# Performance work log

Hardware: AMD Instinct MI355X
Metric: run time of the kernel (lower is better)

Reference implementation:

```python
import jax, jax.numpy as jnp
import numpy as np

N_X, N_U, N_Y = 256, 32, 32
BATCH, T = 16, 8192
LAM_MIN, LAM_MAX = 0.9, 0.995
B_SCALE, D_SCALE = 0.25, 0.25


def setup_inputs() -> dict:
    key = jax.random.key(0)
    k = jax.random.split(key, 6)
    # Orthogonal Q via QR of a random Gaussian matrix (as in the torch module)
    M = jax.random.normal(k[0], (N_X, N_X), dtype=jnp.float32)
    Q, _ = jnp.linalg.qr(M)
    lam = LAM_MIN + (LAM_MAX - LAM_MIN) * jax.random.uniform(k[1], (N_X,), dtype=jnp.float32)
    Bmat = B_SCALE * jax.random.normal(k[2], (N_X, N_U), dtype=jnp.float32)
    # C picks out the first n_y coordinates (C[i, i] = 1)
    C = jnp.eye(N_Y, N_X, dtype=jnp.float32)
    D = D_SCALE * jax.random.normal(k[3], (N_Y, N_U), dtype=jnp.float32)
    x0 = jax.random.normal(k[4], (BATCH, N_X), dtype=jnp.float32)
    u = jax.random.normal(k[5], (BATCH, T, N_U), dtype=jnp.float32)
    return {"x0": x0, "u": u, "Q": Q, "lam": lam, "Bmat": Bmat, "C": C, "D": D}


def _diag_scan(lam, v):
    """Diagonal linear recurrence x_t = lam * x_{t-1} + v_t (x_0 folded into v[:, 0]).

    lam: (N,), v: (B, T, N) -> states x_1..x_T of shape (B, T, N).
    """
    a = jnp.broadcast_to(lam, v.shape)

    def op(l, r):
        a1, b1 = l
        a2, b2 = r
        return a1 * a2, a2 * b1 + b2

    return jax.lax.associative_scan(op, (a, v), axis=1)[1]


def reference(x0, u, Q, lam, Bmat, C, D):
    Bz = Q.T @ Bmat            # (n_x, n_u) modal input matrix
    Cz = C @ Q                 # (n_y, n_x) modal output matrix
    z0 = x0 @ Q                # (B, n_x)   modal initial state
    v = jnp.einsum('btu,nu->btn', u, Bz)   # (B, T, n_x)
    v = v.at[:, 0].add(lam * z0)            # fold lam * z0 into first step
    z_next = _diag_scan(lam, v)             # (B, T, n_x) = z_1..z_T
    # y_t uses z_t for t = 0..T-1 (states[:, :-1] in the original)
    z_prev = jnp.concatenate([z0[:, None, :], z_next[:, :-1]], axis=1)
    y = jnp.einsum('btn,yn->bty', z_prev, Cz) + jnp.einsum('btu,yu->bty', u, D)
    return y
```

## Files before the change

kernel.cpp:

```cpp
#include <hip/hip_runtime.h>

typedef _Float16 half4_t __attribute__((ext_vector_type(4)));
typedef _Float16 half8_t __attribute__((ext_vector_type(8)));
typedef float f32x4 __attribute__((ext_vector_type(4)));

constexpr int NX = 256, NU = 32, NY = 32, BATCH = 16, T = 8192;
constexpr int NC = 64, L = 128;
constexpr int SUBT = 32, NSUB = L / SUBT;
constexpr int KW = NX + NU;
constexpr int VP = 40;
constexpr int ZP = 264;
constexpr int POOLSZ = NX * VP;

__global__ __launch_bounds__(256) void k_pre(
    const float* __restrict__ x0, const float* __restrict__ Q,
    const float* __restrict__ Bm, const float* __restrict__ C,
    const float* __restrict__ D,
    _Float16* __restrict__ Bzh, _Float16* __restrict__ Wh, float* __restrict__ z0)
{
    int o = blockIdx.x * 64 + (threadIdx.x >> 2);
    int p = threadIdx.x & 3;
    if (o >= 20480) {
        if (p == 0) {
            int g = o - 20480, iy = g >> 5, j = g & 31;
            Wh[iy * KW + NX + j] = (_Float16)D[iy * NU + j];
        }
        return;
    }
    float s = 0.f;
    int k0 = p * 64;
    if (o < 8192) {
        int n = o >> 5, j = o & 31;
        for (int k = k0; k < k0 + 64; ++k) s = fmaf(Q[k * NX + n], Bm[k * NU + j], s);
    } else if (o < 16384) {
        int g = o - 8192; int iy = g >> 8, nn = g & 255;
        for (int k = k0; k < k0 + 64; ++k) s = fmaf(C[iy * NX + k], Q[k * NX + nn], s);
    } else {
        int g = o - 16384; int b = g >> 8, nn = g & 255;
        for (int k = k0; k < k0 + 64; ++k) s = fmaf(x0[b * NX + k], Q[k * NX + nn], s);
    }
    s += __shfl_xor(s, 1);
    s += __shfl_xor(s, 2);
    if (p == 0) {
        if (o < 8192) {
            Bzh[o] = (_Float16)s;
        } else if (o < 16384) {
            int g = o - 8192; int iy = g >> 8, nn = g & 255;
            Wh[iy * KW + nn] = (_Float16)s;
        } else {
            z0[o - 16384] = s;
        }
    }
}

__global__ __launch_bounds__(256) void k_phase1(
    const float* __restrict__ u, const float* __restrict__ lam,
    const _Float16* __restrict__ Bzh, float* __restrict__ S)
{
    __shared__ __align__(16) _Float16 ut[2][SUBT][32];

    const int b = blockIdx.x >> 6, c = blockIdx.x & 63, tid = threadIdx.x;
    const int w = tid >> 6, lane = tid & 63, m16 = lane & 15, quad = lane >> 4;

    half8_t bfrag[4];
    #pragma unroll
    for (int i = 0; i < 4; ++i)
        bfrag[i] = *(const half8_t*)&Bzh[((4 * w + i) * 16 + m16) * NU + quad * 8];

    float wr[4][4], wt16[4], l32[4], acc[4];
    #pragma unroll
    for (int i = 0; i < 4; ++i) {
        float la = lam[(4 * w + i) * 16 + m16];
        float p2 = la * la, p4 = p2 * p2, p8 = p4 * p4, p16 = p8 * p8;
        float inv1 = 1.0f / la;
        float inv4 = (inv1 * inv1) * (inv1 * inv1);
        float pq = 1.0f;
        if (quad & 1) pq *= inv4;
        if (quad & 2) pq *= inv4 * inv4;
        float w0 = (p16 * p8 * p4 * p2 * la) * pq;
        wr[i][0] = w0;
        wr[i][1] = w0 * inv1;
        wr[i][2] = wr[i][1] * inv1;
        wr[i][3] = wr[i][2] * inv1;
        wt16[i] = 1.0f / p16;
        l32[i] = p16 * p16;
        acc[i] = 0.f;
    }

    const float* ug = u + ((size_t)(b * T) + (size_t)c * L) * NU;

    for (int sub = 0; sub < NSUB; ++sub) {
        {
            float4 uu = *(const float4*)(ug + (size_t)sub * SUBT * NU + tid * 4);
            int tr = tid >> 3, cb = ((tid & 7) * 4 + (tr & 3) * 8) & 31;
            half4_t h; h.x = (_Float16)uu.x; h.y = (_Float16)uu.y;
            h.z = (_Float16)uu.z; h.w = (_Float16)uu.w;
            *(half4_t*)&ut[sub & 1][tr][cb] = h;
        }
        __syncthreads();
        int rot = (m16 & 3) * 8;
        half8_t af0 = *(const half8_t*)&ut[sub & 1][m16][(quad * 8 + rot) & 31];
        half8_t af1 = *(const half8_t*)&ut[sub & 1][16 + m16][(quad * 8 + rot) & 31];
        #pragma unroll
        for (int i = 0; i < 4; ++i) {
            f32x4 z4 = {0.f, 0.f, 0.f, 0.f};
            f32x4 v0 = __builtin_amdgcn_mfma_f32_16x16x32_f16(af0, bfrag[i], z4, 0, 0, 0);
            f32x4 v1 = __builtin_amdgcn_mfma_f32_16x16x32_f16(af1, bfrag[i], z4, 0, 0, 0);
            float s0 = wr[i][0] * v0[0] + wr[i][1] * v0[1] + wr[i][2] * v0[2] + wr[i][3] * v0[3];
            float s1 = wr[i][0] * v1[0] + wr[i][1] * v1[1] + wr[i][2] * v1[2] + wr[i][3] * v1[3];
            acc[i] = fmaf(l32[i], acc[i], fmaf(wt16[i], s1, s0));
        }
    }
    #pragma unroll
    for (int i = 0; i < 4; ++i) {
        acc[i] += __shfl_xor(acc[i], 16);
        acc[i] += __shfl_xor(acc[i], 32);
    }
    float out = quad == 0 ? acc[0] : quad == 1 ? acc[1] : quad == 2 ? acc[2] : acc[3];
    S[(size_t)blockIdx.x * NX + (4 * w + quad) * 16 + m16] = out;
}

__global__ __launch_bounds__(256) void k_phase3(
    const float* __restrict__ u, const float* __restrict__ lam,
    const _Float16* __restrict__ Bzh, const _Float16* __restrict__ Wh,
    const float* __restrict__ S, const float* __restrict__ z0,
    float* __restrict__ y)
{
    __shared__ __align__(16) _Float16 ut[2][SUBT][32];
    __shared__ __align__(16) _Float16 pool[POOLSZ];
    __shared__ float pvec[NX];

    const int b = blockIdx.x >> 6, c = blockIdx.x & 63, tid = threadIdx.x;
    const int w = tid >> 6, lane = tid & 63, m16 = lane & 15, quad = lane >> 4;
    const int tw = w & 1, yw = w >> 1;

    {
        float la = lam[tid], lamL = la;
        #pragma unroll
        for (int i = 0; i < 7; ++i) lamL *= lamL;
        const float* Sb = S + (size_t)(b * NC) * NX;
        float pv = 0.f, wgt = 1.f;
        for (int cc = c - 1; cc >= 0; --cc) {
            pv = fmaf(wgt, Sb[(size_t)cc * NX + tid], pv);
            wgt *= lamL;
        }
        pvec[tid] = fmaf(wgt, z0[b * NX + tid], pv);
    }

    half8_t bfrag[4];
    #pragma unroll
    for (int i = 0; i < 4; ++i)
        bfrag[i] = *(const half8_t*)&Bzh[((4 * w + i) * 16 + m16) * NU + quad * 8];
    half8_t wfrag[9];
    #pragma unroll
    for (int kk = 0; kk < 9; ++kk)
        wfrag[kk] = *(const half8_t*)&Wh[(yw * 16 + m16) * KW + kk * 32 + quad * 8];
    half8_t triA[2];
    #pragma unroll
    for (int tt = 0; tt < 2; ++tt) {
        #pragma unroll
        for (int j = 0; j < 8; ++j)
            triA[tt][j] = (_Float16)((quad * 8 + j < tt * 16 + m16) ? 1.f : 0.f);
    }

    float lamn[4], inv1[4], iq[4], i16p[4], fq[4], f16p[4], l32[4], p[4];
    #pragma unroll
    for (int i = 0; i < 4; ++i) {
        int ni = (4 * w + i) * 16 + m16;
        float la = lam[ni];
        lamn[i] = la;
        float p2 = la * la, p4 = p2 * p2, p8 = p4 * p4, p16 = p8 * p8;
        float iv = 1.0f / la;
        inv1[i] = iv;
        float iv4 = (iv * iv) * (iv * iv);
        float pqi = 1.0f, pqf = 1.0f;
        if (quad & 1) { pqi *= iv4; pqf *= p4; }
        if (quad & 2) { pqi *= iv4 * iv4; pqf *= p8; }
        iq[i] = iv * pqi;
        fq[i] = pqf;
        i16p[i] = 1.0f / p16;
        f16p[i] = p16;
        l32[i] = p16 * p16;
    }
    __syncthreads();
    #pragma unroll
    for (int i = 0; i < 4; ++i)
        p[i] = pvec[(4 * w + i) * 16 + m16];

    const float* ug = u + ((size_t)(b * T) + (size_t)c * L) * NU;
    float* yg = y + ((size_t)(b * T) + (size_t)c * L) * NY;
    const int rot = (m16 & 3) * 8;

    for (int sub = 0; sub < NSUB; ++sub) {
        {
            float4 uu = *(const float4*)(ug + (size_t)sub * SUBT * NU + tid * 4);
            int tr = tid >> 3, cb = ((tid & 7) * 4 + (tr & 3) * 8) & 31;
            half4_t h; h.x = (_Float16)uu.x; h.y = (_Float16)uu.y;
            h.z = (_Float16)uu.z; h.w = (_Float16)uu.w;
            *(half4_t*)&ut[sub & 1][tr][cb] = h;
        }
        __syncthreads();

        half8_t af0 = *(const half8_t*)&ut[sub & 1][m16][(quad * 8 + rot) & 31];
        half8_t af1 = *(const half8_t*)&ut[sub & 1][16 + m16][(quad * 8 + rot) & 31];
        float partial[4];
        #pragma unroll
        for (int i = 0; i < 4; ++i) {
            int ni = (4 * w + i) * 16 + m16;
            f32x4 z4 = {0.f, 0.f, 0.f, 0.f};
            f32x4 v0 = __builtin_amdgcn_mfma_f32_16x16x32_f16(af0, bfrag[i], z4, 0, 0, 0);
            f32x4 v1 = __builtin_amdgcn_mfma_f32_16x16x32_f16(af1, bfrag[i], z4, 0, 0, 0);
            float ps = 0.f;
            float sc = iq[i];
            half4_t h0, h1;
            #pragma unroll
            for (int r = 0; r < 4; ++r) {
                float a0 = v0[r] * sc;
                float a1 = v1[r] * (sc * i16p[i]);
                ps += a0 + a1;
                h0[r] = (_Float16)a0;
                h1[r] = (_Float16)a1;
                sc *= inv1[i];
            }
            partial[i] = ps;
            *(half4_t*)&pool[ni * VP + quad * 4] = h0;
            *(half4_t*)&pool[ni * VP + 16 + quad * 4] = h1;
        }
        __syncthreads();

        f32x4 zp0[4], zp1[4];
        #pragma unroll
        for (int i = 0; i < 4; ++i) {
            int ni = (4 * w + i) * 16 + m16;
            half8_t bV = *(const half8_t*)&pool[ni * VP + quad * 8];
            f32x4 z4 = {0.f, 0.f, 0.f, 0.f};
            zp0[i] = __builtin_amdgcn_mfma_f32_16x16x32_f16(triA[0], bV, z4, 0, 0, 0);
            zp1[i] = __builtin_amdgcn_mfma_f32_16x16x32_f16(triA[1], bV, z4, 0, 0, 0);
        }
        __syncthreads();

        #pragma unroll
        for (int i = 0; i < 4; ++i) {
            int ni = (4 * w + i) * 16 + m16;
            float f = fq[i];
            #pragma unroll
            for (int r = 0; r < 4; ++r) {
                float zv0 = f * (p[i] + zp0[i][r]);
                float zv1 = (f * f16p[i]) * (p[i] + zp1[i][r]);
                pool[(quad * 4 + r) * ZP + ni] = (_Float16)zv0;
                pool[(16 + quad * 4 + r) * ZP + ni] = (_Float16)zv1;
                f *= lamn[i];
            }
        }
        #pragma unroll
        for (int i = 0; i < 4; ++i) {
            float ps = partial[i];
            ps += __shfl_xor(ps, 16);
            ps += __shfl_xor(ps, 32);
            p[i] = l32[i] * (p[i] + ps);
        }
        __syncthreads();

        f32x4 acc = {0.f, 0.f, 0.f, 0.f};
        #pragma unroll
        for (int kk = 0; kk < 8; ++kk) {
            half8_t az = *(const half8_t*)&pool[(tw * 16 + m16) * ZP + kk * 32 + quad * 8];
            acc = __builtin_amdgcn_mfma_f32_16x16x32_f16(az, wfrag[kk], acc, 0, 0, 0);
        }
        {
            half8_t au = *(const half8_t*)&ut[sub & 1][tw * 16 + m16][(quad * 8 + rot) & 31];
            acc = __builtin_amdgcn_mfma_f32_16x16x32_f16(au, wfrag[8], acc, 0, 0, 0);
        }
        #pragma unroll
        for (int r = 0; r < 4; ++r)
            yg[(size_t)(sub * SUBT + tw * 16 + quad * 4 + r) * NY + yw * 16 + m16] = acc[r];
    }
}

extern "C" void kernel_launch(void* const* d_in, const int* in_sizes, int n_in,
                              void* d_out, int out_size, void* d_ws, size_t ws_size,
                              hipStream_t stream) {
    (void)in_sizes; (void)n_in; (void)out_size; (void)ws_size;
    const float* x0  = (const float*)d_in[0];
    const float* u   = (const float*)d_in[1];
    const float* Q   = (const float*)d_in[2];
    const float* lam = (const float*)d_in[3];
    const float* Bm  = (const float*)d_in[4];
    const float* C   = (const float*)d_in[5];
    const float* D   = (const float*)d_in[6];
    float* y = (float*)d_out;

    char* ws = (char*)d_ws;
    _Float16* Bzh = (_Float16*)(ws);
    _Float16* Wh  = (_Float16*)(ws + 16384);
    float*    z0  = (float*)(ws + 34816);
    float*    S   = (float*)(ws + 51200);

    k_pre   <<<336, 256, 0, stream>>>(x0, Q, Bm, C, D, Bzh, Wh, z0);
    k_phase1<<<BATCH * NC, 256, 0, stream>>>(u, lam, Bzh, S);
    k_phase3<<<BATCH * NC, 256, 0, stream>>>(u, lam, Bzh, Wh, S, z0, y);
}
```

Baseline: 129.9 us.

## Replace triangular-MFMA prefix sum with register/shuffle scan and exp2 carry weights

```diff
diff --git a/kernel.cpp b/kernel.cpp
--- a/kernel.cpp
+++ b/kernel.cpp
@@ -8,9 +8,7 @@
 constexpr int NC = 64, L = 128;
 constexpr int SUBT = 32, NSUB = L / SUBT;
 constexpr int KW = NX + NU;
-constexpr int VP = 40;
 constexpr int ZP = 264;
-constexpr int POOLSZ = NX * VP;
 
 __global__ __launch_bounds__(256) void k_pre(
     const float* __restrict__ x0, const float* __restrict__ Q,
@@ -127,7 +125,7 @@
     float* __restrict__ y)
 {
     __shared__ __align__(16) _Float16 ut[2][SUBT][32];
-    __shared__ __align__(16) _Float16 pool[POOLSZ];
+    __shared__ __align__(16) _Float16 zt[SUBT][ZP];
     __shared__ float pvec[NX];
 
     const int b = blockIdx.x >> 6, c = blockIdx.x & 63, tid = threadIdx.x;
@@ -135,16 +133,16 @@
     const int tw = w & 1, yw = w >> 1;
 
     {
-        float la = lam[tid], lamL = la;
-        #pragma unroll
-        for (int i = 0; i < 7; ++i) lamL *= lamL;
-        const float* Sb = S + (size_t)(b * NC) * NX;
-        float pv = 0.f, wgt = 1.f;
-        for (int cc = c - 1; cc >= 0; --cc) {
-            pv = fmaf(wgt, Sb[(size_t)cc * NX + tid], pv);
-            wgt *= lamL;
-        }
-        pvec[tid] = fmaf(wgt, z0[b * NX + tid], pv);
+        float la = lam[tid];
+        float l2L = 128.0f * __log2f(la);
+        const float* Sb = S + (size_t)(b * NC) * NX + tid;
+        float pv = 0.f;
+        #pragma unroll 8
+        for (int k = 0; k < c; ++k) {
+            float wgt = exp2f((float)k * l2L);
+            pv = fmaf(wgt, Sb[(size_t)(c - 1 - k) * NX], pv);
+        }
+        pvec[tid] = fmaf(exp2f((float)c * l2L), z0[b * NX + tid], pv);
     }
 
     half8_t bfrag[4];
@@ -155,13 +153,6 @@
     #pragma unroll
     for (int kk = 0; kk < 9; ++kk)
         wfrag[kk] = *(const half8_t*)&Wh[(yw * 16 + m16) * KW + kk * 32 + quad * 8];
-    half8_t triA[2];
-    #pragma unroll
-    for (int tt = 0; tt < 2; ++tt) {
-        #pragma unroll
-        for (int j = 0; j < 8; ++j)
-            triA[tt][j] = (_Float16)((quad * 8 + j < tt * 16 + m16) ? 1.f : 0.f);
-    }
 
     float lamn[4], inv1[4], iq[4], i16p[4], fq[4], f16p[4], l32[4], p[4];
     #pragma unroll
@@ -203,68 +194,52 @@
 
         half8_t af0 = *(const half8_t*)&ut[sub & 1][m16][(quad * 8 + rot) & 31];
         half8_t af1 = *(const half8_t*)&ut[sub & 1][16 + m16][(quad * 8 + rot) & 31];
-        float partial[4];
         #pragma unroll
         for (int i = 0; i < 4; ++i) {
             int ni = (4 * w + i) * 16 + m16;
             f32x4 z4 = {0.f, 0.f, 0.f, 0.f};
             f32x4 v0 = __builtin_amdgcn_mfma_f32_16x16x32_f16(af0, bfrag[i], z4, 0, 0, 0);
             f32x4 v1 = __builtin_amdgcn_mfma_f32_16x16x32_f16(af1, bfrag[i], z4, 0, 0, 0);
-            float ps = 0.f;
+            float a0[4], a1[4];
             float sc = iq[i];
-            half4_t h0, h1;
             #pragma unroll
             for (int r = 0; r < 4; ++r) {
-                float a0 = v0[r] * sc;
-                float a1 = v1[r] * (sc * i16p[i]);
-                ps += a0 + a1;
-                h0[r] = (_Float16)a0;
-                h1[r] = (_Float16)a1;
+                a0[r] = v0[r] * sc;
+                a1[r] = v1[r] * (sc * i16p[i]);
                 sc *= inv1[i];
             }
-            partial[i] = ps;
-            *(half4_t*)&pool[ni * VP + quad * 4] = h0;
-            *(half4_t*)&pool[ni * VP + 16 + quad * 4] = h1;
-        }
-        __syncthreads();
-
-        f32x4 zp0[4], zp1[4];
-        #pragma unroll
-        for (int i = 0; i < 4; ++i) {
-            int ni = (4 * w + i) * 16 + m16;
-            half8_t bV = *(const half8_t*)&pool[ni * VP + quad * 8];
-            f32x4 z4 = {0.f, 0.f, 0.f, 0.f};
-            zp0[i] = __builtin_amdgcn_mfma_f32_16x16x32_f16(triA[0], bV, z4, 0, 0, 0);
-            zp1[i] = __builtin_amdgcn_mfma_f32_16x16x32_f16(triA[1], bV, z4, 0, 0, 0);
-        }
-        __syncthreads();
-
-        #pragma unroll
-        for (int i = 0; i < 4; ++i) {
-            int ni = (4 * w + i) * 16 + m16;
+            float e0[4], e1[4];
+            e0[0] = 0.f; e0[1] = a0[0]; e0[2] = e0[1] + a0[1]; e0[3] = e0[2] + a0[2];
+            float S40 = e0[3] + a0[3];
+            e1[0] = 0.f; e1[1] = a1[0]; e1[2] = e1[1] + a1[1]; e1[3] = e1[2] + a1[2];
+            float S41 = e1[3] + a1[3];
+            float incl0 = S40;
+            float t0 = __shfl_up(incl0, 16); if (quad >= 1) incl0 += t0;
+            t0 = __shfl_up(incl0, 32);       if (quad >= 2) incl0 += t0;
+            float excl0 = incl0 - S40;
+            float total0 = __shfl(incl0, 48 + m16);
+            float incl1 = S41;
+            float t1 = __shfl_up(incl1, 16); if (quad >= 1) incl1 += t1;
+            t1 = __shfl_up(incl1, 32);       if (quad >= 2) incl1 += t1;
+            float excl1 = incl1 - S41;
+            float total1 = __shfl(incl1, 48 + m16);
             float f = fq[i];
             #pragma unroll
             for (int r = 0; r < 4; ++r) {
-                float zv0 = f * (p[i] + zp0[i][r]);
-                float zv1 = (f * f16p[i]) * (p[i] + zp1[i][r]);
-                pool[(quad * 4 + r) * ZP + ni] = (_Float16)zv0;
-                pool[(16 + quad * 4 + r) * ZP + ni] = (_Float16)zv1;
+                float zv0 = f * (p[i] + (excl0 + e0[r]));
+                float zv1 = (f * f16p[i]) * (p[i] + (total0 + excl1 + e1[r]));
+                zt[quad * 4 + r][ni] = (_Float16)zv0;
+                zt[16 + quad * 4 + r][ni] = (_Float16)zv1;
                 f *= lamn[i];
             }
-        }
-        #pragma unroll
-        for (int i = 0; i < 4; ++i) {
-            float ps = partial[i];
-            ps += __shfl_xor(ps, 16);
-            ps += __shfl_xor(ps, 32);
-            p[i] = l32[i] * (p[i] + ps);
+            p[i] = l32[i] * (p[i] + (total0 + total1));
         }
         __syncthreads();
 
         f32x4 acc = {0.f, 0.f, 0.f, 0.f};
         #pragma unroll
         for (int kk = 0; kk < 8; ++kk) {
-            half8_t az = *(const half8_t*)&pool[(tw * 16 + m16) * ZP + kk * 32 + quad * 8];
+            half8_t az = *(const half8_t*)&zt[tw * 16 + m16][kk * 32 + quad * 8];
             acc = __builtin_amdgcn_mfma_f32_16x16x32_f16(az, wfrag[kk], acc, 0, 0, 0);
         }
         {
```

After: 118.6 us. 1.1x faster.
